# Kernel optimization log

Hardware: AMD Instinct MI355X
Metric: run time of the kernel (lower is better)

## Reference

```python
import jax, jax.numpy as jnp
import numpy as np

TOT_LEN, MEM_LEN, BSZ = 1024, 1024, 4
SEG_LEN = TOT_LEN + MEM_LEN
D_EMBED, N_HEAD, D_HEAD = 1024, 16, 64


def setup_inputs() -> dict:
    key = jax.random.key(0)
    ks = jax.random.split(key, 8)
    sc = 0.02
    w = jax.random.normal(ks[0], (TOT_LEN, BSZ, D_EMBED), jnp.float32)
    r = jax.random.normal(ks[1], (SEG_LEN, D_EMBED), jnp.float32)
    r_w_bias = jax.random.normal(ks[2], (N_HEAD, D_HEAD), jnp.float32) * sc
    r_r_bias = jax.random.normal(ks[3], (N_HEAD, D_HEAD), jnp.float32) * sc
    mems = jax.random.normal(ks[4], (MEM_LEN, BSZ, D_EMBED), jnp.float32)
    Wqkv = jax.random.normal(ks[5], (D_EMBED, 3 * N_HEAD * D_HEAD), jnp.float32) * sc
    Wr = jax.random.normal(ks[6], (D_EMBED, N_HEAD * D_HEAD), jnp.float32) * sc
    Wo = jax.random.normal(ks[7], (N_HEAD * D_HEAD, D_EMBED), jnp.float32) * sc
    # causal mask: query i may attend to keys j <= i + MEM_LEN; True = disallow
    i = jnp.arange(TOT_LEN)[:, None]
    j = jnp.arange(SEG_LEN)[None, :]
    attn_mask = (j > i + MEM_LEN)[:, :, None]  # (tot_len, seg_len, 1) bool
    return {"w": w, "r": r, "r_w_bias": r_w_bias, "r_r_bias": r_r_bias,
            "attn_mask": attn_mask, "mems": mems, "Wqkv": Wqkv, "Wr": Wr, "Wo": Wo}


def _rel_shift(x):
    # x: (i, j, b, n) -> Transformer-XL relative shift
    i, j, b, n = x.shape
    x = jnp.pad(x, ((0, 0), (1, 0), (0, 0), (0, 0)))  # zero-pad along j
    x = x.reshape(j + 1, i, b, n)[1:].reshape(i, j, b, n)
    return x


def reference(w, r, r_w_bias, r_r_bias, attn_mask, mems, Wqkv, Wr, Wo):
    tot_len, bsz, _ = w.shape
    seg_len = r.shape[0]
    scale = 1.0 / (D_HEAD ** 0.5)
    cat = jnp.concatenate([mems, w], axis=0)            # (S, b, E)
    w_heads = cat @ Wqkv                                 # (S, b, 3*H*D)
    q, k, v = jnp.split(w_heads, 3, axis=-1)
    q = q[-tot_len:].reshape(tot_len, bsz, N_HEAD, D_HEAD)
    k = k.reshape(seg_len, bsz, N_HEAD, D_HEAD)
    v = v.reshape(seg_len, bsz, N_HEAD, D_HEAD)
    r_head_k = (r @ Wr).reshape(seg_len, N_HEAD, D_HEAD)
    AC = jnp.einsum('ibnd,jbnd->ijbn', q + r_w_bias, k)
    BD = jnp.einsum('ibnd,jnd->ijbn', q + r_r_bias, r_head_k)
    BD = _rel_shift(BD)
    attn_score = (AC + BD) * scale                       # (i, j, b, n)
    attn_score = jnp.where(attn_mask[:, :, :, None], -jnp.inf, attn_score)
    attn_prob = jax.nn.softmax(attn_score, axis=1)
    attn_vec = jnp.einsum('ijbn,jbnd->ibnd', attn_prob, v)
    attn_vec = attn_vec.reshape(tot_len, bsz, N_HEAD * D_HEAD)
    return attn_vec @ Wo
```

## Files before the change

### kernel.cpp

```cpp
#include <hip/hip_runtime.h>
#include <cstddef>


static constexpr int kTot = 1024;
static constexpr int kMem = 1024;
static constexpr int kSeg = 2048;
static constexpr int kBsz = 4;
static constexpr int kEmb = 1024;
static constexpr int kNH  = 16;
static constexpr int kDH  = 64;

typedef __attribute__((ext_vector_type(8))) short bf16x8;
typedef __attribute__((ext_vector_type(4))) float f32x4;
typedef unsigned short ushort_t;

__device__ __forceinline__ ushort_t f2bf(float f) {
    union { float f; unsigned u; } v; v.f = f;
    unsigned r = v.u + 0x7fffu + ((v.u >> 16) & 1u);
    return (ushort_t)(r >> 16);
}

__device__ __forceinline__ void gl_lds16(const ushort_t* g, ushort_t* l) {
    __builtin_amdgcn_global_load_lds(
        (const __attribute__((address_space(1))) unsigned int*)g,
        (__attribute__((address_space(3))) unsigned int*)l, 16, 0, 0);
}

__global__ __launch_bounds__(256) void cvt_bf16_kernel(
    const float* __restrict__ src, ushort_t* __restrict__ dst, int n8)
{
    const int i = blockIdx.x * 256 + threadIdx.x;
    if (i >= n8) return;
    const float4 a = ((const float4*)src)[2 * i];
    const float4 b = ((const float4*)src)[2 * i + 1];
    ushort_t o[8] = {f2bf(a.x), f2bf(a.y), f2bf(a.z), f2bf(a.w),
                     f2bf(b.x), f2bf(b.y), f2bf(b.z), f2bf(b.w)};
    *(uint4*)(dst + (size_t)i * 8) = *(const uint4*)o;
}

__global__ __launch_bounds__(256) void transpose_cvt_kernel(
    const float* __restrict__ src, ushort_t* __restrict__ dst, int K, int N)
{
    __shared__ ushort_t Ts[64][72];
    const int t  = threadIdx.x;
    const int n0 = blockIdx.x * 64;
    const int k0 = blockIdx.y * 64;
#pragma unroll
    for (int g2 = 0; g2 < 4; ++g2) {
        const int kl  = (t >> 4) + g2 * 16;
        const int nl4 = (t & 15) * 4;
        const float4 v = *(const float4*)(src + (size_t)(k0 + kl) * N + n0 + nl4);
        Ts[nl4 + 0][kl] = f2bf(v.x);
        Ts[nl4 + 1][kl] = f2bf(v.y);
        Ts[nl4 + 2][kl] = f2bf(v.z);
        Ts[nl4 + 3][kl] = f2bf(v.w);
    }
    __syncthreads();
    const int nl = t >> 2;
    const int c  = (t & 3) * 16;
    ushort_t tmp[16];
#pragma unroll
    for (int e = 0; e < 16; ++e) tmp[e] = Ts[nl][c + e];
    ushort_t* drow = dst + (size_t)(n0 + nl) * K + k0 + c;
    *(uint4*)drow       = *(const uint4*)tmp;
    *(uint4*)(drow + 8) = *(const uint4*)(tmp + 8);
}

template<int MODE>
__global__ __launch_bounds__(256) void gemm_bf16_kernel(
    const ushort_t* __restrict__ A, const ushort_t* __restrict__ B,
    float* __restrict__ outq, ushort_t* __restrict__ outk, ushort_t* __restrict__ outv)
{
    __shared__ ushort_t Al[128 * 64];
    __shared__ ushort_t Bl[128 * 64];

    const int t    = threadIdx.x;
    const int lane = t & 63;
    const int w    = t >> 6;
    const int c15  = lane & 15;
    const int g    = lane >> 4;
    const int wr   = w >> 1;
    const int wc   = w & 1;
    const int n0   = blockIdx.x * 128;
    const int m0   = blockIdx.y * 128;

    const int srow = t >> 3;
    const int scc  = t & 7;
    const int wbase = (t & ~63);

    const f32x4 z4 = {0.f, 0.f, 0.f, 0.f};
    f32x4 acc[4][4];
#pragma unroll
    for (int mb = 0; mb < 4; ++mb)
#pragma unroll
        for (int nb = 0; nb < 4; ++nb) acc[mb][nb] = z4;

    for (int k0 = 0; k0 < kEmb; k0 += 64) {
        __syncthreads();
        const ushort_t* Ab = A + (size_t)m0 * kEmb + k0;
        const ushort_t* Bb = B + (size_t)n0 * kEmb + k0;
#pragma unroll
        for (int q = 0; q < 4; ++q) {
            const int row  = q * 32 + srow;
            const int gcol = scc ^ (row & 7);
            gl_lds16(Ab + (size_t)row * kEmb + gcol * 8, Al + (q * 256 + wbase) * 8);
            gl_lds16(Bb + (size_t)row * kEmb + gcol * 8, Bl + (q * 256 + wbase) * 8);
        }
        __syncthreads();
#pragma unroll
        for (int ks = 0; ks < 2; ++ks) {
            bf16x8 af[4], bfr[4];
#pragma unroll
            for (int mb = 0; mb < 4; ++mb) {
                const int row = wr * 64 + mb * 16 + c15;
                af[mb] = *(const bf16x8*)((const char*)Al + row * 128 +
                           ((ks * 64 + g * 16) ^ ((row & 7) << 4)));
            }
#pragma unroll
            for (int nb = 0; nb < 4; ++nb) {
                const int row = wc * 64 + nb * 16 + c15;
                bfr[nb] = *(const bf16x8*)((const char*)Bl + row * 128 +
                            ((ks * 64 + g * 16) ^ ((row & 7) << 4)));
            }
#pragma unroll
            for (int mb = 0; mb < 4; ++mb)
#pragma unroll
                for (int nb = 0; nb < 4; ++nb)
                    acc[mb][nb] = __builtin_amdgcn_mfma_f32_16x16x32_bf16(
                        af[mb], bfr[nb], acc[mb][nb], 0, 0, 0);
        }
    }

#pragma unroll
    for (int mb = 0; mb < 4; ++mb) {
#pragma unroll
        for (int ri = 0; ri < 4; ++ri) {
            const int gm = m0 + wr * 64 + mb * 16 + g * 4 + ri;
#pragma unroll
            for (int nb = 0; nb < 4; ++nb) {
                const int gn    = n0 + wc * 64 + nb * 16 + c15;
                const float val = acc[mb][nb][ri];
                if (MODE == 0) {
                    const int s = gm >> 2, b = gm & 3;
                    const int part = gn >> 10, within = gn & 1023;
                    const int hn = within >> 6, d = within & 63;
                    if (part == 0) {
                        if (s >= kMem)
                            outq[(((size_t)(b * kNH + hn) * kTot + (s - kMem)) << 6) + d] = val;
                    } else if (part == 1) {
                        outk[(((size_t)(b * kNH + hn) * kSeg + s) << 6) + d] = f2bf(val);
                    } else {
                        outv[(((size_t)(b * kNH + hn) * kSeg + s) << 6) + d] = f2bf(val);
                    }
                } else {
                    const int hn = gn >> 6, d = gn & 63;
                    outk[(((size_t)hn * kSeg + gm) << 6) + d] = f2bf(val);
                }
            }
        }
    }
}

__global__ __launch_bounds__(256) void gemm_out_kernel(
    const float* __restrict__ av, const float* __restrict__ Wo,
    float* __restrict__ out)
{
    __shared__ float As[16][68];
    __shared__ float Bs[16][68];
    const int t  = threadIdx.x;
    const int m0 = blockIdx.x * 64;
    const int n0 = blockIdx.y * 64;
    const int r0 = (t & 15) * 4;
    const int c0 = (t >> 4) * 4;
    const int lm = t >> 2;
    const int k4 = t & 3;
    const int lk  = t >> 4;
    const int ln4 = t & 15;
    const float* arow = av + (size_t)(m0 + lm) * kEmb;

    float acc[4][4] = {};
    for (int k0 = 0; k0 < kEmb; k0 += 16) {
        const float4 a  = *(const float4*)(arow + k0 + k4 * 4);
        const float4 bv = *(const float4*)(Wo + (size_t)(k0 + lk) * 1024 + n0 + ln4 * 4);
        __syncthreads();
        As[k4 * 4 + 0][lm] = a.x;
        As[k4 * 4 + 1][lm] = a.y;
        As[k4 * 4 + 2][lm] = a.z;
        As[k4 * 4 + 3][lm] = a.w;
        *(float4*)&Bs[lk][ln4 * 4] = bv;
        __syncthreads();
#pragma unroll
        for (int kk = 0; kk < 16; ++kk) {
            const float4 av4 = *(const float4*)&As[kk][r0];
            const float4 b4  = *(const float4*)&Bs[kk][c0];
            const float ar[4] = {av4.x, av4.y, av4.z, av4.w};
            const float br[4] = {b4.x, b4.y, b4.z, b4.w};
#pragma unroll
            for (int x = 0; x < 4; ++x)
#pragma unroll
                for (int y = 0; y < 4; ++y)
                    acc[x][y] = fmaf(ar[x], br[y], acc[x][y]);
        }
    }

#pragma unroll
    for (int x = 0; x < 4; ++x) {
        const int gm = m0 + r0 + x;
#pragma unroll
        for (int y = 0; y < 4; ++y) {
            out[(size_t)gm * 1024 + n0 + c0 + y] = acc[x][y];
        }
    }
}

__global__ __launch_bounds__(256, 4) void attn_kernel(
    const float* __restrict__ q_ws, const ushort_t* __restrict__ k_bf,
    const ushort_t* __restrict__ v_bf, const ushort_t* __restrict__ r_bf,
    const float* __restrict__ rwb, const float* __restrict__ rrb,
    float* __restrict__ av_ws)
{
    __shared__ char lds[40960];
    char* Kl = lds;
    char* Rl = lds + 8192;
    char* Vl = lds + 24576;
    char* Pl = lds + 32768;

    const int t    = threadIdx.x;
    const int lane = t & 63;
    const int w    = t >> 6;
    const int c15  = lane & 15;
    const int g    = lane >> 4;
    const int swz  = (c15 & 7) << 4;

    const int xr   = blockIdx.x;
    const int iblk = (xr & 1) ? (15 - (xr >> 1)) : (xr >> 1);
    const int i0   = iblk << 6;
    const int h    = blockIdx.y;
    const int b    = h >> 4, n = h & 15;
    const int iw0  = i0 + w * 16;

    const float*    qbase = q_ws + ((size_t)h * kTot << 6);
    const ushort_t* kbase = k_bf + ((size_t)h * kSeg << 6);
    const ushort_t* vbase = v_bf + ((size_t)h * kSeg << 6);
    const ushort_t* rbase = r_bf + ((size_t)n * kSeg << 6);

    bf16x8 qw[2], qr[2];
    {
        const float* qrow = qbase + ((size_t)(iw0 + c15) << 6);
        const float* wb = rwb + n * 64;
        const float* rb = rrb + n * 64;
#pragma unroll
        for (int ks = 0; ks < 2; ++ks) {
            const int d0 = ks * 32 + g * 8;
#pragma unroll
            for (int e = 0; e < 8; ++e) {
                const float qv = qrow[d0 + e];
                qw[ks][e] = (short)f2bf(qv + wb[d0 + e]);
                qr[ks][e] = (short)f2bf(qv + rb[d0 + e]);
            }
        }
    }

    const f32x4 z4 = {0.f, 0.f, 0.f, 0.f};
    f32x4 o[4] = {z4, z4, z4, z4};
    float m_run[4] = {-1e30f, -1e30f, -1e30f, -1e30f};
    float l_run[4] = {0.f, 0.f, 0.f, 0.f};

    const int ntiles = (i0 + 1151) >> 6;
    for (int tile = 0; tile < ntiles; ++tile) {
        const int j0 = tile << 6;
        const int relbase = j0 - i0 + 960;

        __syncthreads();

        {
            const int jrow = t >> 2, dq = t & 3;
            const ushort_t* src = kbase + (((size_t)(j0 + jrow)) << 6) + dq * 16;
            const uint4 a0 = ((const uint4*)src)[0];
            const uint4 a1 = ((const uint4*)src)[1];
            const int rs = (jrow & 7) << 4;
            const int colA = dq << 5;
            *(uint4*)(Kl + (jrow << 7) + (colA ^ rs))        = a0;
            *(uint4*)(Kl + (jrow << 7) + ((colA + 16) ^ rs)) = a1;
        }
        {
            const int row = t >> 1, hf = t & 1;
            const int rel = relbase + row;
            uint4 rv0 = {0,0,0,0}, rv1 = rv0, rv2 = rv0, rv3 = rv0;
            if (rel < kSeg) {
                const ushort_t* src = rbase + ((size_t)rel << 6) + hf * 32;
                rv0 = ((const uint4*)src)[0]; rv1 = ((const uint4*)src)[1];
                rv2 = ((const uint4*)src)[2]; rv3 = ((const uint4*)src)[3];
            }
            const int rs = (row & 7) << 4;
            char* base = Rl + (row << 7);
            const int cb = hf << 6;
            *(uint4*)(base + ((cb +  0) ^ rs)) = rv0;
            *(uint4*)(base + ((cb + 16) ^ rs)) = rv1;
            *(uint4*)(base + ((cb + 32) ^ rs)) = rv2;
            *(uint4*)(base + ((cb + 48) ^ rs)) = rv3;
        }
        {
            const int j = t & 63, dq = t >> 6;
            const ushort_t* src = vbase + (((size_t)(j0 + j)) << 6) + dq * 16;
            ushort_t tmp[16];
            *(uint4*)tmp       = ((const uint4*)src)[0];
            *(uint4*)(tmp + 8) = ((const uint4*)src)[1];
#pragma unroll
            for (int e = 0; e < 16; ++e) {
                const int d = dq * 16 + e;
                *(ushort_t*)(Vl + (d << 7) + ((j << 1) ^ ((d & 7) << 4))) = tmp[e];
            }
        }
        __syncthreads();

        f32x4 ac[4] = {z4, z4, z4, z4};
#pragma unroll
        for (int nb = 0; nb < 4; ++nb) {
#pragma unroll
            for (int ks = 0; ks < 2; ++ks) {
                const int row = nb * 16 + c15;
                const bf16x8 kf = *(const bf16x8*)(Kl + (row << 7) +
                                   (((ks << 6) | (g << 4)) ^ swz));
                ac[nb] = __builtin_amdgcn_mfma_f32_16x16x32_bf16(qw[ks], kf, ac[nb], 0, 0, 0);
            }
        }
        f32x4 bd[5] = {z4, z4, z4, z4, z4};
        const int rw0 = 48 - 16 * w;
#pragma unroll
        for (int cb = 0; cb < 5; ++cb) {
#pragma unroll
            for (int ks = 0; ks < 2; ++ks) {
                const int row = rw0 + cb * 16 + c15;
                const bf16x8 rf = *(const bf16x8*)(Rl + (row << 7) +
                                   (((ks << 6) | (g << 4)) ^ swz));
                bd[cb] = __builtin_amdgcn_mfma_f32_16x16x32_bf16(qr[ks], rf, bd[cb], 0, 0, 0);
            }
        }

        float s[4][4];
#pragma unroll
        for (int nb = 0; nb < 4; ++nb) {
#pragma unroll
            for (int r = 0; r < 4; ++r) {
                const int sh   = 15 - 4 * g - r;
                const int idx  = c15 + sh;
                const int srcl = (lane & 48) | (idx & 15);
                const float lo = __shfl(bd[nb][r],     srcl);
                const float hi = __shfl(bd[nb + 1][r], srcl);
                const float bdv = (idx >= 16) ? hi : lo;
                const float sv  = (ac[nb][r] + bdv) * 0.125f;
                const int j     = j0 + nb * 16 + c15;
                const int irow  = iw0 + 4 * g + r;
                s[nb][r] = (j <= irow + kMem) ? sv : -1e30f;
            }
        }

        const int pbase = (w << 11);
#pragma unroll
        for (int r = 0; r < 4; ++r) {
            float mt = fmaxf(fmaxf(s[0][r], s[1][r]), fmaxf(s[2][r], s[3][r]));
            mt = fmaxf(mt, __shfl_xor(mt, 1));
            mt = fmaxf(mt, __shfl_xor(mt, 2));
            mt = fmaxf(mt, __shfl_xor(mt, 4));
            mt = fmaxf(mt, __shfl_xor(mt, 8));
            const float mnew = fmaxf(m_run[r], mt);
            const float al   = __expf(m_run[r] - mnew);
            float p[4], ls = 0.f;
#pragma unroll
            for (int nb = 0; nb < 4; ++nb) { p[nb] = __expf(s[nb][r] - mnew); ls += p[nb]; }
            ls += __shfl_xor(ls, 1);
            ls += __shfl_xor(ls, 2);
            ls += __shfl_xor(ls, 4);
            ls += __shfl_xor(ls, 8);
            l_run[r] = l_run[r] * al + ls;
            m_run[r] = mnew;
            const int il = 4 * g + r;
            const int isw = (il & 7) << 4;
#pragma unroll
            for (int nb = 0; nb < 4; ++nb) {
                o[nb][r] *= al;
                *(ushort_t*)(Pl + pbase + (il << 7) +
                             (((nb << 5) + (c15 << 1)) ^ isw)) = f2bf(p[nb]);
            }
        }

        bf16x8 pf[2];
#pragma unroll
        for (int ks = 0; ks < 2; ++ks)
            pf[ks] = *(const bf16x8*)(Pl + pbase + (c15 << 7) +
                       (((ks << 6) | (g << 4)) ^ swz));
#pragma unroll
        for (int nb = 0; nb < 4; ++nb) {
#pragma unroll
            for (int ks = 0; ks < 2; ++ks) {
                const int row = nb * 16 + c15;
                const bf16x8 vf = *(const bf16x8*)(Vl + (row << 7) +
                                   (((ks << 6) | (g << 4)) ^ swz));
                o[nb] = __builtin_amdgcn_mfma_f32_16x16x32_bf16(pf[ks], vf, o[nb], 0, 0, 0);
            }
        }
    }

#pragma unroll
    for (int r = 0; r < 4; ++r) {
        const float inv = 1.0f / l_run[r];
        const int irow  = iw0 + 4 * g + r;
#pragma unroll
        for (int nb = 0; nb < 4; ++nb) {
            av_ws[(((size_t)(irow * 4 + b)) << 10) + n * 64 + nb * 16 + c15] =
                o[nb][r] * inv;
        }
    }
}


extern "C" void kernel_launch(void* const* d_in, const int* in_sizes, int n_in,
                              void* d_out, int out_size, void* d_ws, size_t ws_size,
                              hipStream_t stream) {
    (void)in_sizes; (void)n_in; (void)out_size; (void)ws_size;

    const float* w    = (const float*)d_in[0];
    const float* r    = (const float*)d_in[1];
    const float* rwb  = (const float*)d_in[2];
    const float* rrb  = (const float*)d_in[3];
    const float* mems = (const float*)d_in[5];
    const float* Wqkv = (const float*)d_in[6];
    const float* Wr   = (const float*)d_in[7];
    const float* Wo   = (const float*)d_in[8];
    float* out = (float*)d_out;

    char* ws = (char*)d_ws;
    ushort_t* cat_bf = (ushort_t*)ws;
    ushort_t* wqkvT  = (ushort_t*)(ws + (16u << 20));
    ushort_t* wrT    = (ushort_t*)(ws + (22u << 20));
    ushort_t* r_a    = (ushort_t*)(ws + (24u << 20));
    float*    q_ws   = (float*)   (ws + (28u << 20));
    ushort_t* k_bf   = (ushort_t*)(ws + (44u << 20));
    ushort_t* v_bf   = (ushort_t*)(ws + (60u << 20));
    ushort_t* r_bf   = (ushort_t*)(ws + (76u << 20));
    float*    av_ws  = (float*)   (ws + (80u << 20));

    cvt_bf16_kernel<<<2048, 256, 0, stream>>>(mems, cat_bf, 524288);
    cvt_bf16_kernel<<<2048, 256, 0, stream>>>(w, cat_bf + 4194304, 524288);
    cvt_bf16_kernel<<<1024, 256, 0, stream>>>(r, r_a, 262144);
    transpose_cvt_kernel<<<dim3(48, 16), 256, 0, stream>>>(Wqkv, wqkvT, 1024, 3072);
    transpose_cvt_kernel<<<dim3(16, 16), 256, 0, stream>>>(Wr, wrT, 1024, 1024);

    gemm_bf16_kernel<0><<<dim3(24, 64), 256, 0, stream>>>(cat_bf, wqkvT, q_ws, k_bf, v_bf);
    gemm_bf16_kernel<1><<<dim3(8, 16), 256, 0, stream>>>(r_a, wrT, nullptr, r_bf, nullptr);

    attn_kernel<<<dim3(16, 64), 256, 0, stream>>>(q_ws, k_bf, v_bf, r_bf, rwb, rrb, av_ws);
    gemm_out_kernel<<<dim3(64, 16), 256, 0, stream>>>(av_ws, Wo, out);
}
```

Before: 545.5 us.

## Use bf16 MFMA for output projection, prefetch attention tiles, merge prep kernels

The FP32 SIMT output-projection GEMM is replaced with the existing bf16 MFMA GEMM in a new output mode. The attention kernel now writes its result in bf16, and Wo is transposed into bf16. In the attention loop, the next K, V and R tiles are loaded into registers while the current tile is computed. R is kept in a rolling double-half LDS layout so only 64 new rows load per tile, and the row-sum reduction is deferred to the end. The conversion and transpose launches are merged into two kernels. Precision drops for the attention output and Wo.

```diff
diff --git a/kernel.cpp b/kernel.cpp
--- a/kernel.cpp
+++ b/kernel.cpp
@@ -26,25 +26,40 @@
         (__attribute__((address_space(3))) unsigned int*)l, 16, 0, 0);
 }
 
-__global__ __launch_bounds__(256) void cvt_bf16_kernel(
-    const float* __restrict__ src, ushort_t* __restrict__ dst, int n8)
+__global__ __launch_bounds__(256) void cvt3_kernel(
+    const float* __restrict__ mems, const float* __restrict__ w,
+    const float* __restrict__ r,
+    ushort_t* __restrict__ cat_bf, ushort_t* __restrict__ r_a)
 {
     const int i = blockIdx.x * 256 + threadIdx.x;
-    if (i >= n8) return;
-    const float4 a = ((const float4*)src)[2 * i];
-    const float4 b = ((const float4*)src)[2 * i + 1];
+    const float* src;
+    ushort_t* dst;
+    if (i < 524288)        { src = mems + (size_t)i * 8;             dst = cat_bf + (size_t)i * 8; }
+    else if (i < 1048576)  { src = w + (size_t)(i - 524288) * 8;     dst = cat_bf + (size_t)i * 8; }
+    else                   { src = r + (size_t)(i - 1048576) * 8;    dst = r_a + (size_t)(i - 1048576) * 8; }
+    const float4 a = ((const float4*)src)[0];
+    const float4 b = ((const float4*)src)[1];
     ushort_t o[8] = {f2bf(a.x), f2bf(a.y), f2bf(a.z), f2bf(a.w),
                      f2bf(b.x), f2bf(b.y), f2bf(b.z), f2bf(b.w)};
-    *(uint4*)(dst + (size_t)i * 8) = *(const uint4*)o;
-}
-
-__global__ __launch_bounds__(256) void transpose_cvt_kernel(
-    const float* __restrict__ src, ushort_t* __restrict__ dst, int K, int N)
+    *(uint4*)dst = *(const uint4*)o;
+}
+
+__global__ __launch_bounds__(256) void transpose3_kernel(
+    const float* __restrict__ Wqkv, const float* __restrict__ Wr,
+    const float* __restrict__ Wo,
+    ushort_t* __restrict__ wqkvT, ushort_t* __restrict__ wrT,
+    ushort_t* __restrict__ woT)
 {
     __shared__ ushort_t Ts[64][72];
+    const int bid = blockIdx.x;
+    const float* src; ushort_t* dst; int N, rel;
+    if (bid < 768)       { src = Wqkv; dst = wqkvT; N = 3072; rel = bid; }
+    else if (bid < 1024) { src = Wr;   dst = wrT;   N = 1024; rel = bid - 768; }
+    else                 { src = Wo;   dst = woT;   N = 1024; rel = bid - 1024; }
+    const int nx = N >> 6;
+    const int n0 = (rel % nx) << 6;
+    const int k0 = (rel / nx) << 6;
     const int t  = threadIdx.x;
-    const int n0 = blockIdx.x * 64;
-    const int k0 = blockIdx.y * 64;
 #pragma unroll
     for (int g2 = 0; g2 < 4; ++g2) {
         const int kl  = (t >> 4) + g2 * 16;
@@ -61,7 +76,7 @@
     ushort_t tmp[16];
 #pragma unroll
     for (int e = 0; e < 16; ++e) tmp[e] = Ts[nl][c + e];
-    ushort_t* drow = dst + (size_t)(n0 + nl) * K + k0 + c;
+    ushort_t* drow = dst + (size_t)(n0 + nl) * 1024 + k0 + c;
     *(uint4*)drow       = *(const uint4*)tmp;
     *(uint4*)(drow + 8) = *(const uint4*)(tmp + 8);
 }
@@ -152,63 +167,13 @@
                     } else {
                         outv[(((size_t)(b * kNH + hn) * kSeg + s) << 6) + d] = f2bf(val);
                     }
-                } else {
+                } else if (MODE == 1) {
                     const int hn = gn >> 6, d = gn & 63;
                     outk[(((size_t)hn * kSeg + gm) << 6) + d] = f2bf(val);
+                } else {
+                    outq[(size_t)gm * 1024 + gn] = val;
                 }
             }
-        }
-    }
-}
-
-__global__ __launch_bounds__(256) void gemm_out_kernel(
-    const float* __restrict__ av, const float* __restrict__ Wo,
-    float* __restrict__ out)
-{
-    __shared__ float As[16][68];
-    __shared__ float Bs[16][68];
-    const int t  = threadIdx.x;
-    const int m0 = blockIdx.x * 64;
-    const int n0 = blockIdx.y * 64;
-    const int r0 = (t & 15) * 4;
-    const int c0 = (t >> 4) * 4;
-    const int lm = t >> 2;
-    const int k4 = t & 3;
-    const int lk  = t >> 4;
-    const int ln4 = t & 15;
-    const float* arow = av + (size_t)(m0 + lm) * kEmb;
-
-    float acc[4][4] = {};
-    for (int k0 = 0; k0 < kEmb; k0 += 16) {
-        const float4 a  = *(const float4*)(arow + k0 + k4 * 4);
-        const float4 bv = *(const float4*)(Wo + (size_t)(k0 + lk) * 1024 + n0 + ln4 * 4);
-        __syncthreads();
-        As[k4 * 4 + 0][lm] = a.x;
-        As[k4 * 4 + 1][lm] = a.y;
-        As[k4 * 4 + 2][lm] = a.z;
-        As[k4 * 4 + 3][lm] = a.w;
-        *(float4*)&Bs[lk][ln4 * 4] = bv;
-        __syncthreads();
-#pragma unroll
-        for (int kk = 0; kk < 16; ++kk) {
-            const float4 av4 = *(const float4*)&As[kk][r0];
-            const float4 b4  = *(const float4*)&Bs[kk][c0];
-            const float ar[4] = {av4.x, av4.y, av4.z, av4.w};
-            const float br[4] = {b4.x, b4.y, b4.z, b4.w};
-#pragma unroll
-            for (int x = 0; x < 4; ++x)
-#pragma unroll
-                for (int y = 0; y < 4; ++y)
-                    acc[x][y] = fmaf(ar[x], br[y], acc[x][y]);
-        }
-    }
-
-#pragma unroll
-    for (int x = 0; x < 4; ++x) {
-        const int gm = m0 + r0 + x;
-#pragma unroll
-        for (int y = 0; y < 4; ++y) {
-            out[(size_t)gm * 1024 + n0 + c0 + y] = acc[x][y];
         }
     }
 }
@@ -217,7 +182,7 @@
     const float* __restrict__ q_ws, const ushort_t* __restrict__ k_bf,
     const ushort_t* __restrict__ v_bf, const ushort_t* __restrict__ r_bf,
     const float* __restrict__ rwb, const float* __restrict__ rrb,
-    float* __restrict__ av_ws)
+    ushort_t* __restrict__ av_bf)
 {
     __shared__ char lds[40960];
     char* Kl = lds;
@@ -261,6 +226,47 @@
         }
     }
 
+    const int jrowK = t >> 2, dqK = t & 3;
+    const int jv = t & 63,  dqv = t >> 6;
+    const int qR = t >> 2,  cR  = t & 3;
+
+    {
+        const ushort_t* src = kbase + ((size_t)jrowK << 6) + dqK * 16;
+        const uint4 a0 = ((const uint4*)src)[0];
+        const uint4 a1 = ((const uint4*)src)[1];
+        const int rs = (jrowK & 7) << 4;
+        const int colA = dqK << 5;
+        *(uint4*)(Kl + (jrowK << 7) + (colA ^ rs))        = a0;
+        *(uint4*)(Kl + (jrowK << 7) + ((colA + 16) ^ rs)) = a1;
+    }
+    {
+        const int row = t >> 1, hf = t & 1;
+        const int rel = 960 - i0 + row;
+        const ushort_t* src = rbase + ((size_t)rel << 6) + hf * 32;
+        const uint4 rv0 = ((const uint4*)src)[0];
+        const uint4 rv1 = ((const uint4*)src)[1];
+        const uint4 rv2 = ((const uint4*)src)[2];
+        const uint4 rv3 = ((const uint4*)src)[3];
+        const int rs = (row & 7) << 4;
+        char* base = Rl + (row << 7);
+        const int cb2 = hf << 6;
+        *(uint4*)(base + ((cb2 +  0) ^ rs)) = rv0;
+        *(uint4*)(base + ((cb2 + 16) ^ rs)) = rv1;
+        *(uint4*)(base + ((cb2 + 32) ^ rs)) = rv2;
+        *(uint4*)(base + ((cb2 + 48) ^ rs)) = rv3;
+    }
+    {
+        const ushort_t* src = vbase + ((size_t)jv << 6) + dqv * 16;
+        ushort_t tmp[16];
+        *(uint4*)tmp       = ((const uint4*)src)[0];
+        *(uint4*)(tmp + 8) = ((const uint4*)src)[1];
+#pragma unroll
+        for (int e = 0; e < 16; ++e) {
+            const int d = dqv * 16 + e;
+            *(ushort_t*)(Vl + (d << 7) + ((jv << 1) ^ ((d & 7) << 4))) = tmp[e];
+        }
+    }
+
     const f32x4 z4 = {0.f, 0.f, 0.f, 0.f};
     f32x4 o[4] = {z4, z4, z4, z4};
     float m_run[4] = {-1e30f, -1e30f, -1e30f, -1e30f};
@@ -268,51 +274,36 @@
 
     const int ntiles = (i0 + 1151) >> 6;
     for (int tile = 0; tile < ntiles; ++tile) {
-        const int j0 = tile << 6;
-        const int relbase = j0 - i0 + 960;
+        const int j0   = tile << 6;
+        const int rxor = (tile & 1) << 6;
 
         __syncthreads();
 
-        {
-            const int jrow = t >> 2, dq = t & 3;
-            const ushort_t* src = kbase + (((size_t)(j0 + jrow)) << 6) + dq * 16;
-            const uint4 a0 = ((const uint4*)src)[0];
-            const uint4 a1 = ((const uint4*)src)[1];
-            const int rs = (jrow & 7) << 4;
-            const int colA = dq << 5;
-            *(uint4*)(Kl + (jrow << 7) + (colA ^ rs))        = a0;
-            *(uint4*)(Kl + (jrow << 7) + ((colA + 16) ^ rs)) = a1;
-        }
-        {
-            const int row = t >> 1, hf = t & 1;
-            const int rel = relbase + row;
-            uint4 rv0 = {0,0,0,0}, rv1 = rv0, rv2 = rv0, rv3 = rv0;
-            if (rel < kSeg) {
-                const ushort_t* src = rbase + ((size_t)rel << 6) + hf * 32;
-                rv0 = ((const uint4*)src)[0]; rv1 = ((const uint4*)src)[1];
-                rv2 = ((const uint4*)src)[2]; rv3 = ((const uint4*)src)[3];
-            }
-            const int rs = (row & 7) << 4;
-            char* base = Rl + (row << 7);
-            const int cb = hf << 6;
-            *(uint4*)(base + ((cb +  0) ^ rs)) = rv0;
-            *(uint4*)(base + ((cb + 16) ^ rs)) = rv1;
-            *(uint4*)(base + ((cb + 32) ^ rs)) = rv2;
-            *(uint4*)(base + ((cb + 48) ^ rs)) = rv3;
-        }
-        {
-            const int j = t & 63, dq = t >> 6;
-            const ushort_t* src = vbase + (((size_t)(j0 + j)) << 6) + dq * 16;
-            ushort_t tmp[16];
-            *(uint4*)tmp       = ((const uint4*)src)[0];
-            *(uint4*)(tmp + 8) = ((const uint4*)src)[1];
-#pragma unroll
-            for (int e = 0; e < 16; ++e) {
-                const int d = dq * 16 + e;
-                *(ushort_t*)(Vl + (d << 7) + ((j << 1) ^ ((d & 7) << 4))) = tmp[e];
-            }
-        }
-        __syncthreads();
+        const bool pf = (tile + 1 < ntiles);
+        uint4 kr0, kr1, vr0, vr1, rr0, rr1;
+        if (pf) {
+            const uint4 z = {0u, 0u, 0u, 0u};
+            kr0 = kr1 = vr0 = vr1 = rr0 = rr1 = z;
+            const int j1 = j0 + 64;
+            const int jK = j1 + jrowK;
+            if (jK < kSeg) {
+                const ushort_t* src = kbase + ((size_t)jK << 6) + dqK * 16;
+                kr0 = ((const uint4*)src)[0];
+                kr1 = ((const uint4*)src)[1];
+            }
+            const int jV = j1 + jv;
+            if (jV < kSeg) {
+                const ushort_t* src = vbase + ((size_t)jV << 6) + dqv * 16;
+                vr0 = ((const uint4*)src)[0];
+                vr1 = ((const uint4*)src)[1];
+            }
+            const int relN = j1 - i0 + 1024 + qR;
+            if (relN < kSeg) {
+                const ushort_t* src = rbase + ((size_t)relN << 6) + cR * 16;
+                rr0 = ((const uint4*)src)[0];
+                rr1 = ((const uint4*)src)[1];
+            }
+        }
 
         f32x4 ac[4] = {z4, z4, z4, z4};
 #pragma unroll
@@ -331,8 +322,9 @@
         for (int cb = 0; cb < 5; ++cb) {
 #pragma unroll
             for (int ks = 0; ks < 2; ++ks) {
-                const int row = rw0 + cb * 16 + c15;
-                const bf16x8 rf = *(const bf16x8*)(Rl + (row << 7) +
+                const int lr = rw0 + cb * 16 + c15;
+                const int pr = lr ^ rxor;
+                const bf16x8 rf = *(const bf16x8*)(Rl + (pr << 7) +
                                    (((ks << 6) | (g << 4)) ^ swz));
                 bd[cb] = __builtin_amdgcn_mfma_f32_16x16x32_bf16(qr[ks], rf, bd[cb], 0, 0, 0);
             }
@@ -340,18 +332,19 @@
 
         float s[4][4];
 #pragma unroll
-        for (int nb = 0; nb < 4; ++nb) {
-#pragma unroll
-            for (int r = 0; r < 4; ++r) {
-                const int sh   = 15 - 4 * g - r;
-                const int idx  = c15 + sh;
-                const int srcl = (lane & 48) | (idx & 15);
-                const float lo = __shfl(bd[nb][r],     srcl);
-                const float hi = __shfl(bd[nb + 1][r], srcl);
-                const float bdv = (idx >= 16) ? hi : lo;
+        for (int r = 0; r < 4; ++r) {
+            const int sh   = 15 - 4 * g - r;
+            const int idx  = c15 + sh;
+            const int srcl = (lane & 48) | (idx & 15);
+            float shv[5];
+#pragma unroll
+            for (int cb = 0; cb < 5; ++cb) shv[cb] = __shfl(bd[cb][r], srcl);
+            const int irow = iw0 + 4 * g + r;
+#pragma unroll
+            for (int nb = 0; nb < 4; ++nb) {
+                const float bdv = (idx >= 16) ? shv[nb + 1] : shv[nb];
                 const float sv  = (ac[nb][r] + bdv) * 0.125f;
                 const int j     = j0 + nb * 16 + c15;
-                const int irow  = iw0 + 4 * g + r;
                 s[nb][r] = (j <= irow + kMem) ? sv : -1e30f;
             }
         }
@@ -366,16 +359,12 @@
             mt = fmaxf(mt, __shfl_xor(mt, 8));
             const float mnew = fmaxf(m_run[r], mt);
             const float al   = __expf(m_run[r] - mnew);
-            float p[4], ls = 0.f;
-#pragma unroll
-            for (int nb = 0; nb < 4; ++nb) { p[nb] = __expf(s[nb][r] - mnew); ls += p[nb]; }
-            ls += __shfl_xor(ls, 1);
-            ls += __shfl_xor(ls, 2);
-            ls += __shfl_xor(ls, 4);
-            ls += __shfl_xor(ls, 8);
-            l_run[r] = l_run[r] * al + ls;
+            float p[4];
+#pragma unroll
+            for (int nb = 0; nb < 4; ++nb) p[nb] = __expf(s[nb][r] - mnew);
+            l_run[r] = l_run[r] * al + (p[0] + p[1]) + (p[2] + p[3]);
             m_run[r] = mnew;
-            const int il = 4 * g + r;
+            const int il  = 4 * g + r;
             const int isw = (il & 7) << 4;
 #pragma unroll
             for (int nb = 0; nb < 4; ++nb) {
@@ -385,11 +374,11 @@
             }
         }
 
-        bf16x8 pf[2];
+        bf16x8 pfr[2];
 #pragma unroll
         for (int ks = 0; ks < 2; ++ks)
-            pf[ks] = *(const bf16x8*)(Pl + pbase + (c15 << 7) +
-                       (((ks << 6) | (g << 4)) ^ swz));
+            pfr[ks] = *(const bf16x8*)(Pl + pbase + (c15 << 7) +
+                        (((ks << 6) | (g << 4)) ^ swz));
 #pragma unroll
         for (int nb = 0; nb < 4; ++nb) {
 #pragma unroll
@@ -397,19 +386,52 @@
                 const int row = nb * 16 + c15;
                 const bf16x8 vf = *(const bf16x8*)(Vl + (row << 7) +
                                    (((ks << 6) | (g << 4)) ^ swz));
-                o[nb] = __builtin_amdgcn_mfma_f32_16x16x32_bf16(pf[ks], vf, o[nb], 0, 0, 0);
+                o[nb] = __builtin_amdgcn_mfma_f32_16x16x32_bf16(pfr[ks], vf, o[nb], 0, 0, 0);
+            }
+        }
+
+        __syncthreads();
+
+        if (pf) {
+            {
+                const int rs = (jrowK & 7) << 4;
+                const int colA = dqK << 5;
+                *(uint4*)(Kl + (jrowK << 7) + (colA ^ rs))        = kr0;
+                *(uint4*)(Kl + (jrowK << 7) + ((colA + 16) ^ rs)) = kr1;
+            }
+            {
+                const int pr = qR ^ rxor;
+                const int rs = (qR & 7) << 4;
+                const int colR = cR << 5;
+                *(uint4*)(Rl + (pr << 7) + (colR ^ rs))        = rr0;
+                *(uint4*)(Rl + (pr << 7) + ((colR + 16) ^ rs)) = rr1;
+            }
+            {
+                ushort_t tmp[16];
+                *(uint4*)tmp       = vr0;
+                *(uint4*)(tmp + 8) = vr1;
+#pragma unroll
+                for (int e = 0; e < 16; ++e) {
+                    const int d = dqv * 16 + e;
+                    *(ushort_t*)(Vl + (d << 7) + ((jv << 1) ^ ((d & 7) << 4))) = tmp[e];
+                }
             }
         }
     }
 
 #pragma unroll
     for (int r = 0; r < 4; ++r) {
-        const float inv = 1.0f / l_run[r];
+        float lsum = l_run[r];
+        lsum += __shfl_xor(lsum, 1);
+        lsum += __shfl_xor(lsum, 2);
+        lsum += __shfl_xor(lsum, 4);
+        lsum += __shfl_xor(lsum, 8);
+        const float inv = 1.0f / lsum;
         const int irow  = iw0 + 4 * g + r;
 #pragma unroll
         for (int nb = 0; nb < 4; ++nb) {
-            av_ws[(((size_t)(irow * 4 + b)) << 10) + n * 64 + nb * 16 + c15] =
-                o[nb][r] * inv;
+            av_bf[(((size_t)(irow * 4 + b)) << 10) + n * 64 + nb * 16 + c15] =
+                f2bf(o[nb][r] * inv);
         }
     }
 }
@@ -439,17 +461,16 @@
     ushort_t* k_bf   = (ushort_t*)(ws + (44u << 20));
     ushort_t* v_bf   = (ushort_t*)(ws + (60u << 20));
     ushort_t* r_bf   = (ushort_t*)(ws + (76u << 20));
-    float*    av_ws  = (float*)   (ws + (80u << 20));
-
-    cvt_bf16_kernel<<<2048, 256, 0, stream>>>(mems, cat_bf, 524288);
-    cvt_bf16_kernel<<<2048, 256, 0, stream>>>(w, cat_bf + 4194304, 524288);
-    cvt_bf16_kernel<<<1024, 256, 0, stream>>>(r, r_a, 262144);
-    transpose_cvt_kernel<<<dim3(48, 16), 256, 0, stream>>>(Wqkv, wqkvT, 1024, 3072);
-    transpose_cvt_kernel<<<dim3(16, 16), 256, 0, stream>>>(Wr, wrT, 1024, 1024);
+    ushort_t* av_bf  = (ushort_t*)(ws + (80u << 20));
+    ushort_t* woT    = (ushort_t*)(ws + (88u << 20));
+
+    cvt3_kernel<<<5120, 256, 0, stream>>>(mems, w, r, cat_bf, r_a);
+    transpose3_kernel<<<1280, 256, 0, stream>>>(Wqkv, Wr, Wo, wqkvT, wrT, woT);
 
     gemm_bf16_kernel<0><<<dim3(24, 64), 256, 0, stream>>>(cat_bf, wqkvT, q_ws, k_bf, v_bf);
     gemm_bf16_kernel<1><<<dim3(8, 16), 256, 0, stream>>>(r_a, wrT, nullptr, r_bf, nullptr);
 
-    attn_kernel<<<dim3(16, 64), 256, 0, stream>>>(q_ws, k_bf, v_bf, r_bf, rwb, rrb, av_ws);
-    gemm_out_kernel<<<dim3(64, 16), 256, 0, stream>>>(av_ws, Wo, out);
-}
+    attn_kernel<<<dim3(16, 64), 256, 0, stream>>>(q_ws, k_bf, v_bf, r_bf, rwb, rrb, av_bf);
+
+    gemm_bf16_kernel<2><<<dim3(8, 32), 256, 0, stream>>>(av_bf, woT, out, nullptr, nullptr);
+}
```

Measured after the change: 583.9 us. 7.0% more time.
